# Performance work log

Hardware: AMD Instinct MI355X
Metric: run time of the kernel (lower is better)

Reference implementation:

```python
import jax, jax.numpy as jnp
import numpy as np

B, T, E, H = 4, 4096, 512, 64

def setup_inputs() -> dict:
    key = jax.random.key(0)
    k1, k2, k3, k4 = jax.random.split(key, 4)
    x = jax.random.normal(k1, (B, T, E), dtype=jnp.float32)
    # nn.Linear(E, H, bias=False) weight has shape [H, E]; y = x @ W.T
    Wq = jax.random.normal(k2, (H, E), dtype=jnp.float32) * (E ** -0.5)
    Wk = jax.random.normal(k3, (H, E), dtype=jnp.float32) * (E ** -0.5)
    Wv = jax.random.normal(k4, (H, E), dtype=jnp.float32) * (E ** -0.5)
    return {"x": x, "Wq": Wq, "Wk": Wk, "Wv": Wv}

def reference(x, Wq, Wk, Wv):
    # projections: [B, T, H]
    q = jnp.einsum('bte,he->bth', x, Wq)
    k = jnp.einsum('bte,he->bth', x, Wk)
    v = jnp.einsum('bte,he->bth', x, Wv)
    scale = 1.0 / jnp.sqrt(jnp.float32(q.shape[-1]))
    scores = jnp.einsum('bth,bsh->bts', q, k) * scale  # [B, T, T]
    t = scores.shape[-1]
    causal = jnp.tril(jnp.ones((t, t), dtype=bool))
    scores = jnp.where(causal, scores, -jnp.inf)
    probs = jax.nn.softmax(scores, axis=-1)
    # dropout p=0.0 (eval) -> identity
    return jnp.einsum('bts,bsh->bth', probs, v)
```

## Files before the change

kernel.cpp:

```cpp
#include <hip/hip_runtime.h>
#include <hip/hip_bf16.h>

#define Bn 4
#define Tn 4096
#define En 512
#define Hn 64
#define NEGINF -3e38f
#define QSCALE 0.1803368801f

typedef __attribute__((ext_vector_type(8))) __bf16 bf16x8;
typedef __attribute__((ext_vector_type(4))) __bf16 bf16x4;
typedef __attribute__((ext_vector_type(4))) float f32x4;

#define MFMA16(a, b, c) __builtin_amdgcn_mfma_f32_16x16x32_bf16(a, b, c, 0, 0, 0)

__device__ __forceinline__ float bf2f(unsigned short u) {
    union { unsigned u; float f; } v; v.u = ((unsigned)u) << 16;
    return v.f;
}
__device__ __forceinline__ unsigned cvtpk(float a, float b) {
    unsigned d;
    asm("v_cvt_pk_bf16_f32 %0, %1, %2" : "=v"(d) : "v"(a), "v"(b));
    return d;
}
__device__ __forceinline__ unsigned short f2bf(float f) {
    union { float f; unsigned u; } v; v.f = f;
    unsigned r = v.u + 0x7fffu + ((v.u >> 16) & 1u);
    return (unsigned short)(r >> 16);
}
__device__ __forceinline__ float exp2fast(float x) {
    float r;
    asm("v_exp_f32 %0, %1" : "=v"(r) : "v"(x));
    return r;
}
__device__ __forceinline__ void gl16(const void* g, void* l) {
    __builtin_amdgcn_global_load_lds(
        (const __attribute__((address_space(1))) unsigned int*)g,
        (__attribute__((address_space(3))) unsigned int*)l, 16, 0, 0);
}

__launch_bounds__(512, 2)
__global__ void proj(const float* __restrict__ x, const float* __restrict__ Wq,
                     const float* __restrict__ Wk, const float* __restrict__ Wv,
                     unsigned short* __restrict__ q16, unsigned short* __restrict__ k16,
                     unsigned short* __restrict__ vt16) {
    __shared__ __align__(16) unsigned char plds[2][32768];
    const int tid = threadIdx.x;
    const int w = tid >> 6, lane = tid & 63, r = lane & 15, g = lane >> 4;
    const int row0 = blockIdx.x * 64;
    const int rsel = (w & 3) * 16, csel = (w >> 2) * 96;

    const int srow = tid >> 3, skc = (tid & 7) * 8;
    const int sby = (tid & 7) * 16;
    f32x4 acc[6];
#pragma unroll
    for (int i = 0; i < 6; ++i) acc[i] = (f32x4){0.f, 0.f, 0.f, 0.f};

    {
        const float4* xp = (const float4*)&x[(row0 + srow) * En + skc];
        float4 f0 = xp[0], f1 = xp[1];
        union { bf16x8 v; unsigned u32[4]; } t;
        t.u32[0] = cvtpk(f0.x, f0.y); t.u32[1] = cvtpk(f0.z, f0.w);
        t.u32[2] = cvtpk(f1.x, f1.y); t.u32[3] = cvtpk(f1.z, f1.w);
        *(bf16x8*)&plds[0][srow * 128 + (sby ^ ((srow & 7) << 4))] = t.v;
#pragma unroll
        for (int i = 0; i < 3; ++i) {
            int chunk = tid + i * 512;
            int wrow = chunk >> 3, kc = (chunk & 7) * 8, by = (chunk & 7) * 16;
            const float* Ws = (wrow < 64) ? &Wq[wrow * En]
                             : (wrow < 128) ? &Wk[(wrow - 64) * En] : &Wv[(wrow - 128) * En];
            const float4* wp = (const float4*)&Ws[kc];
            float4 w0 = wp[0], w1 = wp[1];
            union { bf16x8 v; unsigned u32[4]; } tw;
            tw.u32[0] = cvtpk(w0.x, w0.y); tw.u32[1] = cvtpk(w0.z, w0.w);
            tw.u32[2] = cvtpk(w1.x, w1.y); tw.u32[3] = cvtpk(w1.z, w1.w);
            *(bf16x8*)&plds[0][8192 + wrow * 128 + (by ^ ((wrow & 7) << 4))] = tw.v;
        }
    }
    __syncthreads();

    for (int s = 0; s < 8; ++s) {
        const int pp = s & 1;
        const bool more = (s < 7);
        float4 nf0, nf1;
        float4 nw0[3], nw1[3];
        if (more) {
            int k1 = (s + 1) * 64;
            const float4* xp = (const float4*)&x[(row0 + srow) * En + k1 + skc];
            nf0 = xp[0]; nf1 = xp[1];
#pragma unroll
            for (int i = 0; i < 3; ++i) {
                int chunk = tid + i * 512;
                int wrow = chunk >> 3, kc = (chunk & 7) * 8;
                const float* Ws = (wrow < 64) ? &Wq[wrow * En]
                                 : (wrow < 128) ? &Wk[(wrow - 64) * En] : &Wv[(wrow - 128) * En];
                const float4* wp = (const float4*)&Ws[k1 + kc];
                nw0[i] = wp[0]; nw1[i] = wp[1];
            }
        }
        {
            const unsigned char* A = &plds[pp][0];
            const unsigned char* W = &plds[pp][8192];
            int arow = rsel + r, asw = (arow & 7) << 4;
            bf16x8 a0 = *(const bf16x8*)&A[arow * 128 + ((g * 16) ^ asw)];
            bf16x8 a1 = *(const bf16x8*)&A[arow * 128 + ((64 + g * 16) ^ asw)];
#pragma unroll
            for (int ct = 0; ct < 6; ++ct) {
                int wrow = csel + ct * 16 + r, wsw = (wrow & 7) << 4;
                bf16x8 b0 = *(const bf16x8*)&W[wrow * 128 + ((g * 16) ^ wsw)];
                bf16x8 b1 = *(const bf16x8*)&W[wrow * 128 + ((64 + g * 16) ^ wsw)];
                acc[ct] = MFMA16(a0, b0, acc[ct]);
                acc[ct] = MFMA16(a1, b1, acc[ct]);
            }
        }
        if (more) {
            unsigned char* D = &plds[pp ^ 1][0];
            union { bf16x8 v; unsigned u32[4]; } t;
            t.u32[0] = cvtpk(nf0.x, nf0.y); t.u32[1] = cvtpk(nf0.z, nf0.w);
            t.u32[2] = cvtpk(nf1.x, nf1.y); t.u32[3] = cvtpk(nf1.z, nf1.w);
            *(bf16x8*)&D[srow * 128 + (sby ^ ((srow & 7) << 4))] = t.v;
#pragma unroll
            for (int i = 0; i < 3; ++i) {
                int chunk = tid + i * 512;
                int wrow = chunk >> 3, by = (chunk & 7) * 16;
                union { bf16x8 v; unsigned u32[4]; } tw;
                tw.u32[0] = cvtpk(nw0[i].x, nw0[i].y); tw.u32[1] = cvtpk(nw0[i].z, nw0[i].w);
                tw.u32[2] = cvtpk(nw1[i].x, nw1[i].y); tw.u32[3] = cvtpk(nw1[i].z, nw1[i].w);
                *(bf16x8*)&D[8192 + wrow * 128 + (by ^ ((wrow & 7) << 4))] = tw.v;
            }
        }
        __syncthreads();
    }
#pragma unroll
    for (int ct = 0; ct < 6; ++ct) {
        int n = csel + ct * 16 + r;
#pragma unroll
        for (int reg = 0; reg < 4; ++reg) {
            int gr = row0 + rsel + g * 4 + reg;
            if (n < 64) {
                q16[gr * 64 + n] = f2bf(acc[ct][reg] * QSCALE);
            } else if (n < 128) {
                k16[gr * 64 + (n - 64)] = f2bf(acc[ct][reg]);
            } else {
                int h = n - 128; int bb = gr >> 12; int t = gr & 4095;
                vt16[((bb * 64 + h) << 12) + t] = f2bf(acc[ct][reg]);
            }
        }
    }
}

__launch_bounds__(256, 4)
__global__ void attnp(const unsigned short* __restrict__ q16, const unsigned short* __restrict__ k16,
                      const unsigned short* __restrict__ vt16,
                      unsigned short* __restrict__ po, float* __restrict__ lp) {
    __shared__ __align__(16) unsigned char lds[2][16384];

    const int tid = threadIdx.x;
    const int w = tid >> 6, lane = tid & 63, r = lane & 15, g = lane >> 4;
    const int bid = blockIdx.x;
    const int page = bid >> 8, idx = bid & 255;
    const int s5 = idx >> 3, b = (idx >> 1) & 3, q1 = idx & 1;
    const int jt = (page & 1) ? s5 : 31 - s5;
    const int piece = ((page & 1) << 2) | ((page >> 1) << 1) | q1;
    const size_t kbase = (size_t)b * Tn;
    const int q0 = jt * 128;
    const int nt = 2 * (jt + 1);
    const int t0 = (piece * nt) >> 3;
    const int tEnd = ((piece + 1) * nt) >> 3;
    const int wq0 = q0 + w * 32;

    const unsigned short* Kb = k16 + kbase * 64;
    const unsigned short* Vb = vt16 + ((size_t)(b * 64) << 12);

    const int srl = lane >> 3, scb = (lane & 7) * 16;

    bf16x8 bq[2][2];
#pragma unroll
    for (int qf = 0; qf < 2; ++qf) {
        const unsigned short* qp = &q16[(kbase + wq0 + qf * 16 + r) * 64 + g * 8];
        bq[qf][0] = *(const bf16x8*)qp;
        bq[qf][1] = *(const bf16x8*)(qp + 32);
    }

    f32x4 o[2][4];
#pragma unroll
    for (int qf = 0; qf < 2; ++qf)
#pragma unroll
        for (int i = 0; i < 4; ++i) o[qf][i] = (f32x4){0.f, 0.f, 0.f, 0.f};
    float l_[2] = {0.f, 0.f};

    if (tEnd > t0) {
        int kv0 = t0 * 64;
        unsigned char* D = &lds[t0 & 1][0];
#pragma unroll
        for (int i = 0; i < 4; ++i) {
            int cc = w * 4 + i;
            if (cc < 8) {
                int row = cc * 8 + srl, sw = (row & 7) << 4;
                gl16((const char*)Kb + (size_t)(kv0 + row) * 128 + (scb ^ sw), D + cc * 1024);
            } else {
                int h = (cc - 8) * 8 + srl, sw = (h & 7) << 4;
                gl16((const char*)Vb + (size_t)h * 8192 + (size_t)kv0 * 2 + (scb ^ sw), D + cc * 1024);
            }
        }
    }

    for (int it = t0; it < tEnd; ++it) {
        const int pp = it & 1;
        asm volatile("s_waitcnt vmcnt(0)" ::: "memory");
        __builtin_amdgcn_s_barrier();
        __builtin_amdgcn_sched_barrier(0);
        if (it + 1 < tEnd) {
            int nkv = (it + 1) * 64;
            unsigned char* D = &lds[pp ^ 1][0];
#pragma unroll
            for (int i = 0; i < 4; ++i) {
                int cc = w * 4 + i;
                if (cc < 8) {
                    int row = cc * 8 + srl, sw = (row & 7) << 4;
                    gl16((const char*)Kb + (size_t)(nkv + row) * 128 + (scb ^ sw), D + cc * 1024);
                } else {
                    int h = (cc - 8) * 8 + srl, sw = (h & 7) << 4;
                    gl16((const char*)Vb + (size_t)h * 8192 + (size_t)nkv * 2 + (scb ^ sw), D + cc * 1024);
                }
            }
        }
        const int kv0 = it * 64;
        if (kv0 <= wq0 + 31) {
            const unsigned char* K = &lds[pp][0];
            const unsigned char* V = &lds[pp][8192];
            f32x4 s4[2][4];
            __builtin_amdgcn_s_setprio(1);
#pragma unroll
            for (int ct = 0; ct < 4; ++ct) {
                int row = ct * 16 + r;
                int base = row * 128, sw = (row & 7) << 4;
                bf16x8 ak0 = *(const bf16x8*)&K[base + ((g * 16) ^ sw)];
                bf16x8 ak1 = *(const bf16x8*)&K[base + ((64 + g * 16) ^ sw)];
#pragma unroll
                for (int qf = 0; qf < 2; ++qf) {
                    f32x4 t = (f32x4){0.f, 0.f, 0.f, 0.f};
                    t = MFMA16(ak0, bq[qf][0], t);
                    t = MFMA16(ak1, bq[qf][1], t);
                    s4[qf][ct] = t;
                }
            }
            if (kv0 + 63 > wq0) {
#pragma unroll
                for (int qf = 0; qf < 2; ++qf) {
                    int qq = wq0 + qf * 16 + r;
#pragma unroll
                    for (int ct = 0; ct < 4; ++ct)
#pragma unroll
                        for (int reg = 0; reg < 4; ++reg) {
                            int kv = kv0 + ct * 16 + g * 4 + reg;
                            if (kv > qq) s4[qf][ct][reg] = NEGINF;
                        }
                }
            }
            union { bf16x8 v; unsigned u32[4]; } pk[2][2];
#pragma unroll
            for (int qf = 0; qf < 2; ++qf) {
#pragma unroll
                for (int ct = 0; ct < 4; ++ct)
#pragma unroll
                    for (int reg = 0; reg < 4; ++reg)
                        s4[qf][ct][reg] = exp2fast(s4[qf][ct][reg]);
                l_[qf] += ((s4[qf][0][0] + s4[qf][0][1]) + (s4[qf][0][2] + s4[qf][0][3])) +
                          ((s4[qf][1][0] + s4[qf][1][1]) + (s4[qf][1][2] + s4[qf][1][3])) +
                          ((s4[qf][2][0] + s4[qf][2][1]) + (s4[qf][2][2] + s4[qf][2][3])) +
                          ((s4[qf][3][0] + s4[qf][3][1]) + (s4[qf][3][2] + s4[qf][3][3]));
#pragma unroll
                for (int kf = 0; kf < 2; ++kf) {
                    pk[qf][kf].u32[0] = cvtpk(s4[qf][kf * 2][0], s4[qf][kf * 2][1]);
                    pk[qf][kf].u32[1] = cvtpk(s4[qf][kf * 2][2], s4[qf][kf * 2][3]);
                    pk[qf][kf].u32[2] = cvtpk(s4[qf][kf * 2 + 1][0], s4[qf][kf * 2 + 1][1]);
                    pk[qf][kf].u32[3] = cvtpk(s4[qf][kf * 2 + 1][2], s4[qf][kf * 2 + 1][3]);
                }
            }
#pragma unroll
            for (int cth = 0; cth < 4; ++cth) {
                int h = cth * 16 + r;
                int vb = h * 128, sw2 = (h & 7) << 4;
#pragma unroll
                for (int kf = 0; kf < 2; ++kf) {
                    int off = kf * 64 + g * 8;
                    union { bf16x8 v; bf16x4 h4[2]; } vv;
                    vv.h4[0] = *(const bf16x4*)&V[vb + (off ^ sw2)];
                    vv.h4[1] = *(const bf16x4*)&V[vb + ((off + 32) ^ sw2)];
                    o[0][cth] = MFMA16(pk[0][kf].v, vv.v, o[0][cth]);
                    o[1][cth] = MFMA16(pk[1][kf].v, vv.v, o[1][cth]);
                }
            }
            __builtin_amdgcn_s_setprio(0);
        }
    }

    const size_t qb = (size_t)piece * 16384 + b * 4096;
#pragma unroll
    for (int qf = 0; qf < 2; ++qf) {
#pragma unroll
        for (int cth = 0; cth < 4; ++cth)
#pragma unroll
            for (int reg = 0; reg < 4; ++reg)
                po[(qb + wq0 + qf * 16 + g * 4 + reg) * 64 + cth * 16 + r] = f2bf(o[qf][cth][reg]);
        lp[(qb + wq0 + qf * 16 + r) * 4 + g] = l_[qf];
    }
}

__global__ void merge(const unsigned short* __restrict__ po, const float* __restrict__ lp,
                      float* __restrict__ out) {
    int t = blockIdx.x * 256 + threadIdx.x;
    int q = t >> 3, c8 = (t & 7) * 8;
    float L = 0.f;
#pragma unroll
    for (int c = 0; c < 8; ++c)
#pragma unroll
        for (int gg = 0; gg < 4; ++gg)
            L += lp[((size_t)c * 16384 + q) * 4 + gg];
    float inv = 1.0f / L;
    float acc[8] = {0.f, 0.f, 0.f, 0.f, 0.f, 0.f, 0.f, 0.f};
#pragma unroll
    for (int c = 0; c < 8; ++c) {
        union { uint4 v; unsigned short u[8]; } ld;
        ld.v = *(const uint4*)&po[((size_t)c * 16384 + q) * 64 + c8];
#pragma unroll
        for (int j = 0; j < 8; ++j) acc[j] += bf2f(ld.u[j]);
    }
    float4* op = (float4*)&out[(size_t)q * 64 + c8];
    op[0] = (float4){acc[0] * inv, acc[1] * inv, acc[2] * inv, acc[3] * inv};
    op[1] = (float4){acc[4] * inv, acc[5] * inv, acc[6] * inv, acc[7] * inv};
}

extern "C" void kernel_launch(void* const* d_in, const int* in_sizes, int n_in,
                              void* d_out, int out_size, void* d_ws, size_t ws_size,
                              hipStream_t stream) {
    const float* x  = (const float*)d_in[0];
    const float* Wq = (const float*)d_in[1];
    const float* Wk = (const float*)d_in[2];
    const float* Wv = (const float*)d_in[3];
    float* out = (float*)d_out;
    char* ws = (char*)d_ws;

    unsigned short* q16 = (unsigned short*)ws;
    unsigned short* k16 = (unsigned short*)(ws + 2097152);
    unsigned short* v16 = (unsigned short*)(ws + 4194304);
    unsigned short* po  = (unsigned short*)(ws + 6291456);
    float*          lp  = (float*)(ws + 23068672);

    hipLaunchKernelGGL(proj, dim3(256), dim3(512), 0, stream, x, Wq, Wk, Wv, q16, k16, v16);
    hipLaunchKernelGGL(attnp, dim3(1024), dim3(256), 0, stream, q16, k16, v16, po, lp);
    hipLaunchKernelGGL(merge, dim3(512), dim3(256), 0, stream, po, lp, out);
}
```

Before: 41.08 us.

## Split projection blocks by output column half to double grid size

The projection kernel now launches 512 blocks of 256 threads instead of 256 blocks of 512. Each block computes one 96-column half of the 192 fused Q/K/V outputs for 64 rows, and each block's shared memory shrinks to hold only its own weight half. The goal is to fill more of the GPU's compute units (256 blocks is close to one per CU) and raise occupancy. The cost is that every x tile is now loaded and converted twice, once per column half.

```diff
diff --git a/kernel.cpp b/kernel.cpp
--- a/kernel.cpp
+++ b/kernel.cpp
@@ -39,42 +39,47 @@
         (__attribute__((address_space(3))) unsigned int*)l, 16, 0, 0);
 }
 
-__launch_bounds__(512, 2)
+__launch_bounds__(256, 4)
 __global__ void proj(const float* __restrict__ x, const float* __restrict__ Wq,
                      const float* __restrict__ Wk, const float* __restrict__ Wv,
                      unsigned short* __restrict__ q16, unsigned short* __restrict__ k16,
                      unsigned short* __restrict__ vt16) {
-    __shared__ __align__(16) unsigned char plds[2][32768];
+    __shared__ __align__(16) unsigned char plds[2][20480];
     const int tid = threadIdx.x;
     const int w = tid >> 6, lane = tid & 63, r = lane & 15, g = lane >> 4;
-    const int row0 = blockIdx.x * 64;
-    const int rsel = (w & 3) * 16, csel = (w >> 2) * 96;
-
-    const int srow = tid >> 3, skc = (tid & 7) * 8;
-    const int sby = (tid & 7) * 16;
+    const int bid = blockIdx.x;
+    const int row0 = (bid >> 1) * 64;
+    const int ch = bid & 1;
+    const int rsel = w * 16;
+
+    const int arow_s = tid >> 2, akc = (tid & 3) * 16;
     f32x4 acc[6];
 #pragma unroll
     for (int i = 0; i < 6; ++i) acc[i] = (f32x4){0.f, 0.f, 0.f, 0.f};
 
     {
-        const float4* xp = (const float4*)&x[(row0 + srow) * En + skc];
-        float4 f0 = xp[0], f1 = xp[1];
-        union { bf16x8 v; unsigned u32[4]; } t;
-        t.u32[0] = cvtpk(f0.x, f0.y); t.u32[1] = cvtpk(f0.z, f0.w);
-        t.u32[2] = cvtpk(f1.x, f1.y); t.u32[3] = cvtpk(f1.z, f1.w);
-        *(bf16x8*)&plds[0][srow * 128 + (sby ^ ((srow & 7) << 4))] = t.v;
-#pragma unroll
-        for (int i = 0; i < 3; ++i) {
-            int chunk = tid + i * 512;
-            int wrow = chunk >> 3, kc = (chunk & 7) * 8, by = (chunk & 7) * 16;
-            const float* Ws = (wrow < 64) ? &Wq[wrow * En]
-                             : (wrow < 128) ? &Wk[(wrow - 64) * En] : &Wv[(wrow - 128) * En];
+        const float4* xp = (const float4*)&x[(row0 + arow_s) * En + akc];
+        float4 f0 = xp[0], f1 = xp[1], f2 = xp[2], f3 = xp[3];
+        union { bf16x8 v; unsigned u32[4]; } t0, t1;
+        t0.u32[0] = cvtpk(f0.x, f0.y); t0.u32[1] = cvtpk(f0.z, f0.w);
+        t0.u32[2] = cvtpk(f1.x, f1.y); t0.u32[3] = cvtpk(f1.z, f1.w);
+        t1.u32[0] = cvtpk(f2.x, f2.y); t1.u32[1] = cvtpk(f2.z, f2.w);
+        t1.u32[2] = cvtpk(f3.x, f3.y); t1.u32[3] = cvtpk(f3.z, f3.w);
+        int sw = (arow_s & 7) << 4;
+        *(bf16x8*)&plds[0][arow_s * 128 + ((akc * 2) ^ sw)] = t0.v;
+        *(bf16x8*)&plds[0][arow_s * 128 + ((akc * 2 + 16) ^ sw)] = t1.v;
+#pragma unroll
+        for (int c = 0; c < 3; ++c) {
+            int wrow = (tid >> 3) + c * 32, kc = (tid & 7) * 8;
+            int gw = ch * 96 + wrow;
+            const float* Ws = (gw < 64) ? &Wq[gw * En]
+                             : (gw < 128) ? &Wk[(gw - 64) * En] : &Wv[(gw - 128) * En];
             const float4* wp = (const float4*)&Ws[kc];
             float4 w0 = wp[0], w1 = wp[1];
             union { bf16x8 v; unsigned u32[4]; } tw;
             tw.u32[0] = cvtpk(w0.x, w0.y); tw.u32[1] = cvtpk(w0.z, w0.w);
             tw.u32[2] = cvtpk(w1.x, w1.y); tw.u32[3] = cvtpk(w1.z, w1.w);
-            *(bf16x8*)&plds[0][8192 + wrow * 128 + (by ^ ((wrow & 7) << 4))] = tw.v;
+            *(bf16x8*)&plds[0][8192 + wrow * 128 + ((kc * 2) ^ ((wrow & 7) << 4))] = tw.v;
         }
     }
     __syncthreads();
@@ -82,20 +87,20 @@
     for (int s = 0; s < 8; ++s) {
         const int pp = s & 1;
         const bool more = (s < 7);
-        float4 nf0, nf1;
+        float4 nf[4];
         float4 nw0[3], nw1[3];
         if (more) {
             int k1 = (s + 1) * 64;
-            const float4* xp = (const float4*)&x[(row0 + srow) * En + k1 + skc];
-            nf0 = xp[0]; nf1 = xp[1];
-#pragma unroll
-            for (int i = 0; i < 3; ++i) {
-                int chunk = tid + i * 512;
-                int wrow = chunk >> 3, kc = (chunk & 7) * 8;
-                const float* Ws = (wrow < 64) ? &Wq[wrow * En]
-                                 : (wrow < 128) ? &Wk[(wrow - 64) * En] : &Wv[(wrow - 128) * En];
+            const float4* xp = (const float4*)&x[(row0 + arow_s) * En + k1 + akc];
+            nf[0] = xp[0]; nf[1] = xp[1]; nf[2] = xp[2]; nf[3] = xp[3];
+#pragma unroll
+            for (int c = 0; c < 3; ++c) {
+                int wrow = (tid >> 3) + c * 32, kc = (tid & 7) * 8;
+                int gw = ch * 96 + wrow;
+                const float* Ws = (gw < 64) ? &Wq[gw * En]
+                                 : (gw < 128) ? &Wk[(gw - 64) * En] : &Wv[(gw - 128) * En];
                 const float4* wp = (const float4*)&Ws[k1 + kc];
-                nw0[i] = wp[0]; nw1[i] = wp[1];
+                nw0[c] = wp[0]; nw1[c] = wp[1];
             }
         }
         {
@@ -106,7 +111,7 @@
             bf16x8 a1 = *(const bf16x8*)&A[arow * 128 + ((64 + g * 16) ^ asw)];
 #pragma unroll
             for (int ct = 0; ct < 6; ++ct) {
-                int wrow = csel + ct * 16 + r, wsw = (wrow & 7) << 4;
+                int wrow = ct * 16 + r, wsw = (wrow & 7) << 4;
                 bf16x8 b0 = *(const bf16x8*)&W[wrow * 128 + ((g * 16) ^ wsw)];
                 bf16x8 b1 = *(const bf16x8*)&W[wrow * 128 + ((64 + g * 16) ^ wsw)];
                 acc[ct] = MFMA16(a0, b0, acc[ct]);
@@ -115,25 +120,28 @@
         }
         if (more) {
             unsigned char* D = &plds[pp ^ 1][0];
-            union { bf16x8 v; unsigned u32[4]; } t;
-            t.u32[0] = cvtpk(nf0.x, nf0.y); t.u32[1] = cvtpk(nf0.z, nf0.w);
-            t.u32[2] = cvtpk(nf1.x, nf1.y); t.u32[3] = cvtpk(nf1.z, nf1.w);
-            *(bf16x8*)&D[srow * 128 + (sby ^ ((srow & 7) << 4))] = t.v;
-#pragma unroll
-            for (int i = 0; i < 3; ++i) {
-                int chunk = tid + i * 512;
-                int wrow = chunk >> 3, by = (chunk & 7) * 16;
+            union { bf16x8 v; unsigned u32[4]; } t0, t1;
+            t0.u32[0] = cvtpk(nf[0].x, nf[0].y); t0.u32[1] = cvtpk(nf[0].z, nf[0].w);
+            t0.u32[2] = cvtpk(nf[1].x, nf[1].y); t0.u32[3] = cvtpk(nf[1].z, nf[1].w);
+            t1.u32[0] = cvtpk(nf[2].x, nf[2].y); t1.u32[1] = cvtpk(nf[2].z, nf[2].w);
+            t1.u32[2] = cvtpk(nf[3].x, nf[3].y); t1.u32[3] = cvtpk(nf[3].z, nf[3].w);
+            int sw = (arow_s & 7) << 4;
+            *(bf16x8*)&D[arow_s * 128 + ((akc * 2) ^ sw)] = t0.v;
+            *(bf16x8*)&D[arow_s * 128 + ((akc * 2 + 16) ^ sw)] = t1.v;
+#pragma unroll
+            for (int c = 0; c < 3; ++c) {
+                int wrow = (tid >> 3) + c * 32, kc = (tid & 7) * 8;
                 union { bf16x8 v; unsigned u32[4]; } tw;
-                tw.u32[0] = cvtpk(nw0[i].x, nw0[i].y); tw.u32[1] = cvtpk(nw0[i].z, nw0[i].w);
-                tw.u32[2] = cvtpk(nw1[i].x, nw1[i].y); tw.u32[3] = cvtpk(nw1[i].z, nw1[i].w);
-                *(bf16x8*)&D[8192 + wrow * 128 + (by ^ ((wrow & 7) << 4))] = tw.v;
+                tw.u32[0] = cvtpk(nw0[c].x, nw0[c].y); tw.u32[1] = cvtpk(nw0[c].z, nw0[c].w);
+                tw.u32[2] = cvtpk(nw1[c].x, nw1[c].y); tw.u32[3] = cvtpk(nw1[c].z, nw1[c].w);
+                *(bf16x8*)&D[8192 + wrow * 128 + ((kc * 2) ^ ((wrow & 7) << 4))] = tw.v;
             }
         }
         __syncthreads();
     }
 #pragma unroll
     for (int ct = 0; ct < 6; ++ct) {
-        int n = csel + ct * 16 + r;
+        int n = ch * 96 + ct * 16 + r;
 #pragma unroll
         for (int reg = 0; reg < 4; ++reg) {
             int gr = row0 + rsel + g * 4 + reg;
@@ -348,7 +356,7 @@
     unsigned short* po  = (unsigned short*)(ws + 6291456);
     float*          lp  = (float*)(ws + 23068672);
 
-    hipLaunchKernelGGL(proj, dim3(256), dim3(512), 0, stream, x, Wq, Wk, Wv, q16, k16, v16);
+    hipLaunchKernelGGL(proj, dim3(512), dim3(256), 0, stream, x, Wq, Wk, Wv, q16, k16, v16);
     hipLaunchKernelGGL(attnp, dim3(1024), dim3(256), 0, stream, q16, k16, v16, po, lp);
     hipLaunchKernelGGL(merge, dim3(512), dim3(256), 0, stream, po, lp, out);
 }
```

After: 43.47 us. 5.8% more time.
